# Performance work log

Hardware: AMD Instinct MI355X
Metric: run time of the kernel (lower is better)

Reference implementation:

```python
import jax, jax.numpy as jnp
import numpy as np

BN_EPS = 1e-5


def setup_inputs() -> dict:
    key = jax.random.key(0)
    ks = jax.random.split(key, 8)
    B, C, H, W_ = 64, 512, 28, 28
    return {
        "x": jax.random.normal(ks[0], (B, C, H, W_), dtype=jnp.float32),
        "rsign_bias": 0.1 * jax.random.normal(ks[1], (C,), dtype=jnp.float32),
        "W": jax.random.normal(ks[2], (C, C), dtype=jnp.float32) * 0.05,  # 1x1 conv weight [out,in]
        "bn_gamma": jnp.ones((C,), dtype=jnp.float32),
        "bn_beta": jnp.zeros((C,), dtype=jnp.float32),
        "bn_mean": 0.1 * jax.random.normal(ks[3], (C,), dtype=jnp.float32),
        "bn_var": jax.random.uniform(ks[4], (C,), dtype=jnp.float32, minval=0.5, maxval=1.5),
        "pr_slope": jax.random.uniform(ks[5], (C,), dtype=jnp.float32, minval=0.1, maxval=0.35),
        "pr_shift": 0.1 * jax.random.normal(ks[6], (C,), dtype=jnp.float32),
        "pr_bias": 0.1 * jax.random.normal(ks[7], (C,), dtype=jnp.float32),
    }


def reference(x, rsign_bias, W, bn_gamma, bn_beta, bn_mean, bn_var,
              pr_slope, pr_shift, pr_bias):
    # x: [B, C, H, W] (NCHW). All params are per-channel [C] except W: [C_out, C_in].
    c = lambda v: v[None, :, None, None]  # broadcast per-channel over NCHW

    # RSign: learnable per-channel shift then binarize (forward = sign)
    a = jnp.sign(x + c(rsign_bias))

    # scaled_sign 1x1 conv: per-output-channel scale = mean(|W|), binarized weight
    scale = jnp.mean(jnp.abs(W), axis=1)          # [C_out]
    Wb = jnp.sign(W) * scale[:, None]             # [C_out, C_in]
    y = jnp.einsum('bchw,oc->bohw', a, Wb)        # 1x1 conv == channel GEMM

    # BatchNorm2d (inference form with running stats)
    bn = c(bn_gamma) * (y - c(bn_mean)) * jax.lax.rsqrt(c(bn_var) + BN_EPS) + c(bn_beta)

    # residual shortcut
    s = bn + x

    # RPReLU: prelu(x - shift) + bias, per-channel learnable slope/shift/bias
    t = s - c(pr_shift)
    out = jnp.where(t > 0, t, c(pr_slope) * t) + c(pr_bias)
    return out
```

## Files before the change

### kernel.cpp

```cpp
#include <hip/hip_runtime.h>
#include <cstdint>

#define C_    512
#define HW_   784
#define B_    64
#define BN_EPS 1e-5f


__global__ __launch_bounds__(64) void precompute_kernel(
    const float* __restrict__ W,
    const float* __restrict__ bn_gamma, const float* __restrict__ bn_beta,
    const float* __restrict__ bn_mean,  const float* __restrict__ bn_var,
    const float* __restrict__ pr_slope, const float* __restrict__ pr_shift,
    const float* __restrict__ pr_bias,
    uint32_t* __restrict__ wbits, float4* __restrict__ params)
{
    const int o    = blockIdx.x;
    const int lane = threadIdx.x;
    const float* wrow = W + (size_t)o * C_;

    float s = 0.f;
    for (int c = lane; c < C_; c += 64) s += fabsf(wrow[c]);
    for (int off = 32; off > 0; off >>= 1) s += __shfl_down(s, off, 64);

    if (lane < 16) {
        uint32_t m = 0;
        const int cbase = lane * 32;
        #pragma unroll
        for (int t = 0; t < 32; ++t) {
            if (wrow[cbase + t] < 0.f) m |= (1u << t);
        }
        wbits[o * 16 + lane] = m;
    }

    if (lane == 0) {
        float scale = s * (1.0f / (float)C_);
        float r  = rsqrtf(bn_var[o] + BN_EPS);
        float A  = bn_gamma[o] * scale * r;
        float B2 = bn_beta[o] - bn_gamma[o] * bn_mean[o] * r;
        params[o] = make_float4(A, B2 - pr_shift[o], pr_slope[o], pr_bias[o]);
    }
}

__global__ __launch_bounds__(1024, 8) void fused_kernel(
    const float* __restrict__ x, const float* __restrict__ rsign_bias,
    const uint32_t* __restrict__ wbits, const float4* __restrict__ params,
    float* __restrict__ out)
{
    __shared__ uint32_t abits[64 * 17];

    const int i  = threadIdx.x;
    const int jj = __builtin_amdgcn_readfirstlane(threadIdx.y);
    const int b  = blockIdx.y;
    const int hw = blockIdx.x * 64 + i;
    const bool valid = (hw < HW_);

    const float* xb = x + (size_t)b * C_ * HW_;
    const int c0 = jj * 32;

    if (valid) {
        uint32_t m = 0;
        #pragma unroll
        for (int t = 0; t < 32; ++t) {
            const int c = c0 + t;
            const float v = xb[(size_t)c * HW_ + hw] + rsign_bias[c];
            if (v < 0.f) m |= (1u << t);
        }
        abits[i * 17 + jj] = m;
    }
    __syncthreads();
    if (!valid) return;

    uint32_t a[16];
    #pragma unroll
    for (int w = 0; w < 16; ++w) a[w] = abits[i * 17 + w];

    float* ob = out + (size_t)b * C_ * HW_;

    #pragma unroll
    for (int oo = 0; oo < 32; ++oo) {
        const int o = c0 + oo;
        const uint32_t* wr = wbits + o * 16;
        int P = 0;
        #pragma unroll
        for (int w = 0; w < 16; ++w) P += __popc(a[w] ^ wr[w]);

        const float4 p = params[o];
        const float Sf = (float)(C_ - 2 * P);
        const float t = fmaf(p.x, Sf, p.y) + xb[(size_t)o * HW_ + hw];
        const float r = fmaf(p.z, fminf(t, 0.f), fmaxf(t, 0.f) + p.w);
        ob[(size_t)o * HW_ + hw] = r;
    }
}

extern "C" void kernel_launch(void* const* d_in, const int* in_sizes, int n_in,
                              void* d_out, int out_size, void* d_ws, size_t ws_size,
                              hipStream_t stream) {
    const float* x          = (const float*)d_in[0];
    const float* rsign_bias = (const float*)d_in[1];
    const float* W          = (const float*)d_in[2];
    const float* bn_gamma   = (const float*)d_in[3];
    const float* bn_beta    = (const float*)d_in[4];
    const float* bn_mean    = (const float*)d_in[5];
    const float* bn_var     = (const float*)d_in[6];
    const float* pr_slope   = (const float*)d_in[7];
    const float* pr_shift   = (const float*)d_in[8];
    const float* pr_bias    = (const float*)d_in[9];
    float* out = (float*)d_out;

    uint32_t* wbits = (uint32_t*)d_ws;
    float4*   params = (float4*)((char*)d_ws + 32768);

    precompute_kernel<<<dim3(C_), dim3(64), 0, stream>>>(
        W, bn_gamma, bn_beta, bn_mean, bn_var, pr_slope, pr_shift, pr_bias,
        wbits, params);

    fused_kernel<<<dim3(13, B_), dim3(64, 16), 0, stream>>>(
        x, rsign_bias, wbits, params, out);
}
```

Baseline: 230.9 us.

## Flatten batch-pixel grid, batch loads, fold constants, use nontemporal stores

Flattens the (batch, pixel) indexing into a single dimension so that 784 blocks of 64 pixels each cover the data exactly, which removes the padded 13th tile and its idle lanes. Blocks shrink to 512 threads, with each thread handling 64 channels. The x loads are grouped into batches of 16 or 8 so more memory requests are in flight. The BN affine is folded so the epilogue needs one fma on the popcount, and outputs are written with nontemporal stores to avoid polluting the cache. In exchange, each thread now holds more registers, and the total thread count per pixel is halved.

```diff
diff --git a/kernel.cpp b/kernel.cpp
--- a/kernel.cpp
+++ b/kernel.cpp
@@ -37,12 +37,14 @@
         float scale = s * (1.0f / (float)C_);
         float r  = rsqrtf(bn_var[o] + BN_EPS);
         float A  = bn_gamma[o] * scale * r;
-        float B2 = bn_beta[o] - bn_gamma[o] * bn_mean[o] * r;
-        params[o] = make_float4(A, B2 - pr_shift[o], pr_slope[o], pr_bias[o]);
+        float A2 = -2.0f * A;
+        float C2 = (float)C_ * A + bn_beta[o] - bn_gamma[o] * bn_mean[o] * r
+                 - pr_shift[o];
+        params[o] = make_float4(A2, C2, pr_slope[o], pr_bias[o]);
     }
 }
 
-__global__ __launch_bounds__(1024, 8) void fused_kernel(
+__global__ __launch_bounds__(512, 8) void fused_kernel(
     const float* __restrict__ x, const float* __restrict__ rsign_bias,
     const uint32_t* __restrict__ wbits, const float4* __restrict__ params,
     float* __restrict__ out)
@@ -51,45 +53,59 @@
 
     const int i  = threadIdx.x;
     const int jj = __builtin_amdgcn_readfirstlane(threadIdx.y);
-    const int b  = blockIdx.y;
-    const int hw = blockIdx.x * 64 + i;
-    const bool valid = (hw < HW_);
 
-    const float* xb = x + (size_t)b * C_ * HW_;
-    const int c0 = jj * 32;
+    const uint32_t pair = (uint32_t)blockIdx.x * 64u + (uint32_t)i;
+    const uint32_t b    = pair / 784u;
+    const uint32_t hw   = pair - b * 784u;
+    const size_t   base = (size_t)b * (C_ * HW_) + hw;
+    const float*   xg   = x + base;
 
-    if (valid) {
-        uint32_t m = 0;
+    const int c0 = jj * 64;
+
+    uint32_t m0 = 0, m1 = 0;
+    #pragma unroll
+    for (int half = 0; half < 4; ++half) {
+        float v[16];
         #pragma unroll
-        for (int t = 0; t < 32; ++t) {
-            const int c = c0 + t;
-            const float v = xb[(size_t)c * HW_ + hw] + rsign_bias[c];
-            if (v < 0.f) m |= (1u << t);
+        for (int t = 0; t < 16; ++t)
+            v[t] = xg[(size_t)(c0 + half * 16 + t) * HW_];
+        #pragma unroll
+        for (int t = 0; t < 16; ++t) {
+            const int c = half * 16 + t;
+            const float s = v[t] + rsign_bias[c0 + c];
+            if (c < 32) { if (s < 0.f) m0 |= (1u << c); }
+            else        { if (s < 0.f) m1 |= (1u << (c - 32)); }
         }
-        abits[i * 17 + jj] = m;
     }
+    abits[i * 17 + 2 * jj]     = m0;
+    abits[i * 17 + 2 * jj + 1] = m1;
     __syncthreads();
-    if (!valid) return;
 
     uint32_t a[16];
     #pragma unroll
     for (int w = 0; w < 16; ++w) a[w] = abits[i * 17 + w];
 
-    float* ob = out + (size_t)b * C_ * HW_;
+    float* og = out + base;
 
     #pragma unroll
-    for (int oo = 0; oo < 32; ++oo) {
-        const int o = c0 + oo;
-        const uint32_t* wr = wbits + o * 16;
-        int P = 0;
+    for (int chunk = 0; chunk < 8; ++chunk) {
+        float xv[8];
         #pragma unroll
-        for (int w = 0; w < 16; ++w) P += __popc(a[w] ^ wr[w]);
+        for (int u = 0; u < 8; ++u)
+            xv[u] = xg[(size_t)(c0 + chunk * 8 + u) * HW_];
+        #pragma unroll
+        for (int u = 0; u < 8; ++u) {
+            const int o = c0 + chunk * 8 + u;
+            const uint32_t* wr = wbits + o * 16;
+            int P = 0;
+            #pragma unroll
+            for (int w = 0; w < 16; ++w) P += __popc(a[w] ^ wr[w]);
 
-        const float4 p = params[o];
-        const float Sf = (float)(C_ - 2 * P);
-        const float t = fmaf(p.x, Sf, p.y) + xb[(size_t)o * HW_ + hw];
-        const float r = fmaf(p.z, fminf(t, 0.f), fmaxf(t, 0.f) + p.w);
-        ob[(size_t)o * HW_ + hw] = r;
+            const float4 p = params[o];
+            const float t = fmaf(p.x, (float)P, p.y + xv[u]);
+            const float r = fmaf(p.z, fminf(t, 0.f), fmaxf(t, 0.f) + p.w);
+            __builtin_nontemporal_store(r, &og[(size_t)o * HW_]);
+        }
     }
 }
 
@@ -108,13 +124,13 @@
     const float* pr_bias    = (const float*)d_in[9];
     float* out = (float*)d_out;
 
-    uint32_t* wbits = (uint32_t*)d_ws;
+    uint32_t* wbits  = (uint32_t*)d_ws;
     float4*   params = (float4*)((char*)d_ws + 32768);
 
     precompute_kernel<<<dim3(C_), dim3(64), 0, stream>>>(
         W, bn_gamma, bn_beta, bn_mean, bn_var, pr_slope, pr_shift, pr_bias,
         wbits, params);
 
-    fused_kernel<<<dim3(13, B_), dim3(64, 16), 0, stream>>>(
+    fused_kernel<<<dim3(784), dim3(64, 8), 0, stream>>>(
         x, rsign_bias, wbits, params, out);
 }
```

Result: slower. 308.6 us (+33.7%).

## Flatten batch-pixel grid, reuse loaded x for residual, fold constants into params

Applied to the files above, without the earlier changes.

The grid is flattened over (batch, pixel) pairs so every 64-wide block is full: 64*784 divides evenly by 64, which removes the partially idle 13th block per batch. Each thread keeps its 32 x values in registers and reuses them for the residual add, so x is no longer read a second time from global memory. The BN affine is folded so the epilogue multiplies the popcount directly, saving an operation per output. The cost is 32 more live registers per thread at 1024-thread blocks, plus a per-thread integer divide.

```diff
diff --git a/kernel.cpp b/kernel.cpp
--- a/kernel.cpp
+++ b/kernel.cpp
@@ -37,8 +37,10 @@
         float scale = s * (1.0f / (float)C_);
         float r  = rsqrtf(bn_var[o] + BN_EPS);
         float A  = bn_gamma[o] * scale * r;
-        float B2 = bn_beta[o] - bn_gamma[o] * bn_mean[o] * r;
-        params[o] = make_float4(A, B2 - pr_shift[o], pr_slope[o], pr_bias[o]);
+        float A2 = -2.0f * A;
+        float C2 = (float)C_ * A + bn_beta[o] - bn_gamma[o] * bn_mean[o] * r
+                 - pr_shift[o];
+        params[o] = make_float4(A2, C2, pr_slope[o], pr_bias[o]);
     }
 }
 
@@ -51,31 +53,33 @@
 
     const int i  = threadIdx.x;
     const int jj = __builtin_amdgcn_readfirstlane(threadIdx.y);
-    const int b  = blockIdx.y;
-    const int hw = blockIdx.x * 64 + i;
-    const bool valid = (hw < HW_);
 
-    const float* xb = x + (size_t)b * C_ * HW_;
+    const uint32_t pair = (uint32_t)blockIdx.x * 64u + (uint32_t)i;
+    const uint32_t b    = pair / 784u;
+    const uint32_t hw   = pair - b * 784u;
+    const size_t   base = (size_t)b * (C_ * HW_) + hw;
+    const float*   xg   = x + base;
+
     const int c0 = jj * 32;
 
-    if (valid) {
-        uint32_t m = 0;
-        #pragma unroll
-        for (int t = 0; t < 32; ++t) {
-            const int c = c0 + t;
-            const float v = xb[(size_t)c * HW_ + hw] + rsign_bias[c];
-            if (v < 0.f) m |= (1u << t);
-        }
-        abits[i * 17 + jj] = m;
+    float xv[32];
+    #pragma unroll
+    for (int t = 0; t < 32; ++t)
+        xv[t] = xg[(size_t)(c0 + t) * HW_];
+
+    uint32_t m = 0;
+    #pragma unroll
+    for (int t = 0; t < 32; ++t) {
+        if (xv[t] + rsign_bias[c0 + t] < 0.f) m |= (1u << t);
     }
+    abits[i * 17 + jj] = m;
     __syncthreads();
-    if (!valid) return;
 
     uint32_t a[16];
     #pragma unroll
     for (int w = 0; w < 16; ++w) a[w] = abits[i * 17 + w];
 
-    float* ob = out + (size_t)b * C_ * HW_;
+    float* og = out + base;
 
     #pragma unroll
     for (int oo = 0; oo < 32; ++oo) {
@@ -86,10 +90,9 @@
         for (int w = 0; w < 16; ++w) P += __popc(a[w] ^ wr[w]);
 
         const float4 p = params[o];
-        const float Sf = (float)(C_ - 2 * P);
-        const float t = fmaf(p.x, Sf, p.y) + xb[(size_t)o * HW_ + hw];
+        const float t = fmaf(p.x, (float)P, p.y + xv[oo]);
         const float r = fmaf(p.z, fminf(t, 0.f), fmaxf(t, 0.f) + p.w);
-        ob[(size_t)o * HW_ + hw] = r;
+        og[(size_t)o * HW_] = r;
     }
 }
 
@@ -108,13 +111,13 @@
     const float* pr_bias    = (const float*)d_in[9];
     float* out = (float*)d_out;
 
-    uint32_t* wbits = (uint32_t*)d_ws;
+    uint32_t* wbits  = (uint32_t*)d_ws;
     float4*   params = (float4*)((char*)d_ws + 32768);
 
     precompute_kernel<<<dim3(C_), dim3(64), 0, stream>>>(
         W, bn_gamma, bn_beta, bn_mean, bn_var, pr_slope, pr_shift, pr_bias,
         wbits, params);
 
-    fused_kernel<<<dim3(13, B_), dim3(64, 16), 0, stream>>>(
+    fused_kernel<<<dim3(784), dim3(64, 16), 0, stream>>>(
         x, rsign_bias, wbits, params, out);
 }
```

Measured after the change: 230.9 us. Within noise of the previous version (+0.0%).
